# Kernel optimization log

Measured on AMD Instinct MI355X. Metric: run time of the kernel, lower is better.

## Reference

```python
import jax, jax.numpy as jnp
import numpy as np

B, L, D, E, V = 8, 256, 512, 64, 1000  # batch, length, input_size, edge_size, vocab


def setup_inputs() -> dict:
    key = jax.random.key(0)
    ks = jax.random.split(key, 16)
    s = 0.05
    inp = {
        "inputs": jax.random.normal(ks[0], (B, L, D), jnp.float32),
        "mains": jax.random.randint(ks[1], (B,), 0, L, jnp.int32),
        "adj1": jax.random.randint(ks[2], (B, L, L), 0, 2).astype(jnp.float32),
        "adj2": jax.random.randint(ks[3], (B, L, L), 0, 2).astype(jnp.float32),
        "edge1": jax.random.randint(ks[4], (B, L, L), 0, V, jnp.int32),
        "edge2": jax.random.randint(ks[5], (B, L, L), 0, V, jnp.int32),
        # parameters (torch Linear convention: W is (out, in), y = x @ W.T + b)
        "emb": jax.random.normal(ks[6], (V, E), jnp.float32) * s,
        "W1": jax.random.normal(ks[7], (E, D + E), jnp.float32) * s,
        "W2": jax.random.normal(ks[8], (D, D + E), jnp.float32) * s,
        "b2": jnp.zeros((D,), jnp.float32),
        "W3": jax.random.normal(ks[9], (E, D + E), jnp.float32) * s,
        "W4": jax.random.normal(ks[10], (D, D + E), jnp.float32) * s,
        "b4": jnp.zeros((D,), jnp.float32),
        "W5": jax.random.normal(ks[11], (D, 2 * D), jnp.float32) * s,
        "b5": jnp.zeros((D,), jnp.float32),
    }
    return inp


def reference(inputs, mains, adj1, adj2, edge1, edge2,
              emb, W1, W2, b2, W3, W4, b4, W5, b5):
    K = 3
    eps = 1e-10
    innum = jnp.sum(adj1 > 0, -1, keepdims=True).astype(inputs.dtype) + eps   # (B,L,1)
    outnum = jnp.sum(adj2 > 0, -1, keepdims=True).astype(inputs.dtype) + eps  # (B,L,1)

    # Edge contribution of sum(adj * cat([hid, edge]), -2) is iteration-invariant:
    # sum_j adj[b,i,j] * emb[edge[b,i,j]] -> compute once.
    e1 = emb[edge1]  # (B,L,L,E)
    e2 = emb[edge2]
    esum1 = jnp.einsum('bij,bije->bie', adj1, e1)  # (B,L,E)
    esum2 = jnp.einsum('bij,bije->bie', adj2, e2)

    hid1 = inputs
    hid2 = inputs
    for _ in range(K):
        # hid part of the masked neighbor sum: sum_j adj[b,i,j] * hid[b,j,:]
        hagg1 = jnp.einsum('bij,bjd->bid', adj1, hid1)                  # (B,L,D)
        agg1 = jnp.concatenate([hagg1, esum1], -1) / innum              # (B,L,D+E)
        h1e = jnp.tanh(agg1 @ W1.T)                                     # (B,L,E)
        hid1 = jnp.tanh(jnp.concatenate([h1e, hid1], -1) @ W2.T + b2)   # (B,L,D)

        hagg2 = jnp.einsum('bij,bjd->bid', adj2, hid2)
        agg2 = jnp.concatenate([hagg2, esum2], -1) / outnum
        h2e = jnp.tanh(agg2 @ W3.T)
        hid2 = jnp.tanh(jnp.concatenate([h2e, hid2], -1) @ W4.T + b4)

    fused = jnp.tanh(jnp.concatenate([hid1, hid2], -1) @ W5.T + b5)     # (B,L,D)
    return fused, fused[jnp.arange(fused.shape[0]), mains]
```

## Files before the change

### kernel.cpp

```cpp
#include <hip/hip_runtime.h>
#include <math.h>

#define B_  8
#define L_  256
#define D_  512
#define E_  64
#define DE_ 576
#define R_  2048
#define RG_ 4096

typedef unsigned short ushortT;
typedef __attribute__((ext_vector_type(8))) short bfrag;
typedef __attribute__((ext_vector_type(4))) float f32x4;

#define MFMA16(a,b,c) __builtin_amdgcn_mfma_f32_16x16x32_bf16(a,b,c,0,0,0)

__device__ inline ushortT f2bf(float x){
  unsigned u = __float_as_uint(x);
  u += 0x7FFFu + ((u >> 16) & 1u);
  return (ushortT)(u >> 16);
}
__device__ inline float bf2f(ushortT h){ return __uint_as_float(((unsigned)h) << 16); }

__global__ __launch_bounds__(256) void k_cvt(
    const float* __restrict__ W1, const float* __restrict__ W3,
    const float* __restrict__ W2, const float* __restrict__ W4,
    const float* __restrict__ W5,
    const float* __restrict__ adj1, const float* __restrict__ adj2,
    ushortT* W1h, ushortT* W1l, ushortT* W3h, ushortT* W3l,
    ushortT* W2h, ushortT* W2l, ushortT* W4h, ushortT* W4l,
    ushortT* W5h, ushortT* W5l, ushortT* adjb)
{
  const float* src; ushortT *dh, *dl; int n;
  switch (blockIdx.y) {
    case 0: src = W1;  dh = W1h; dl = W1l; n = 36864;  break;
    case 1: src = W3;  dh = W3h; dl = W3l; n = 36864;  break;
    case 2: src = W2;  dh = W2h; dl = W2l; n = 294912; break;
    case 3: src = W4;  dh = W4h; dl = W4l; n = 294912; break;
    case 4: src = W5;  dh = W5h; dl = W5l; n = 524288; break;
    case 5: src = adj1; dh = adjb;          dl = 0; n = 524288; break;
    default: src = adj2; dh = adjb + 524288; dl = 0; n = 524288; break;
  }
  int i4 = blockIdx.x * 256 + threadIdx.x;
  if (i4 * 4 >= n) return;
  float4 v = ((const float4*)src)[i4];
  float xs[4] = {v.x, v.y, v.z, v.w};
  ushortT h[4], lo[4];
  #pragma unroll
  for (int i = 0; i < 4; ++i) {
    h[i] = f2bf(xs[i]);
    lo[i] = f2bf(xs[i] - bf2f(h[i]));
  }
  ((ushort4*)dh)[i4] = make_ushort4(h[0], h[1], h[2], h[3]);
  if (dl) ((ushort4*)dl)[i4] = make_ushort4(lo[0], lo[1], lo[2], lo[3]);
}

__global__ __launch_bounds__(256) void k_precompute(
    const float* __restrict__ adj1, const float* __restrict__ adj2,
    const int* __restrict__ edge1, const int* __restrict__ edge2,
    const float* __restrict__ emb,
    ushortT* __restrict__ esumh, ushortT* __restrict__ esuml,
    float* __restrict__ num)
{
  int g = blockIdx.x >> 11;
  int r = blockIdx.x & 2047;
  const float* adj  = (g ? adj2 : adj1) + (size_t)r * L_;
  const int*   edge = (g ? edge2 : edge1) + (size_t)r * L_;
  const float4* emb4 = (const float4*)emb;

  int t = threadIdx.x;
  int e4 = t & 15, jc = t >> 4;
  float4 acc = {0.f, 0.f, 0.f, 0.f};
  float cnt = 0.f;
  #pragma unroll
  for (int k = 0; k < 16; ++k) {
    int j = jc * 16 + k;
    float a = adj[j];
    if (a != 0.0f) {
      int id = edge[j];
      float4 e = emb4[(size_t)id * 16 + e4];
      acc.x += a * e.x; acc.y += a * e.y; acc.z += a * e.z; acc.w += a * e.w;
      if (e4 == 0 && a > 0.0f) cnt += 1.0f;
    }
  }

  __shared__ float4 red[16][16];
  __shared__ float cred[16];
  red[jc][e4] = acc;
  if (e4 == 0) cred[jc] = cnt;
  __syncthreads();
  for (int s = 8; s > 0; s >>= 1) {
    if (jc < s) {
      float4 o = red[jc + s][e4];
      float4 m = red[jc][e4];
      m.x += o.x; m.y += o.y; m.z += o.z; m.w += o.w;
      red[jc][e4] = m;
    }
    __syncthreads();
  }
  if (t < 16) {
    float4 v = red[0][t];
    float xs[4] = {v.x, v.y, v.z, v.w};
    size_t base = ((size_t)g * R_ + r) * 64 + t * 4;
    #pragma unroll
    for (int i = 0; i < 4; ++i) {
      ushortT hi = f2bf(xs[i]);
      esumh[base + i] = hi;
      esuml[base + i] = f2bf(xs[i] - bf2f(hi));
    }
  }
  if (t == 0) {
    float c = 0.f;
    #pragma unroll
    for (int q = 0; q < 16; ++q) c += cred[q];
    num[g * R_ + r] = c + 1e-10f;
  }
}

__global__ __launch_bounds__(256) void k_init_hid(
    const float* __restrict__ inp, ushortT* __restrict__ hh, ushortT* __restrict__ hl)
{
  int idx = blockIdx.x * 256 + threadIdx.x;
  float4 v = ((const float4*)inp)[idx];
  float xs[4] = {v.x, v.y, v.z, v.w};
  ushortT h[4], lo[4];
  #pragma unroll
  for (int i = 0; i < 4; ++i) {
    h[i] = f2bf(xs[i]);
    lo[i] = f2bf(xs[i] - bf2f(h[i]));
  }
  ushort4 vh = make_ushort4(h[0], h[1], h[2], h[3]);
  ushort4 vl = make_ushort4(lo[0], lo[1], lo[2], lo[3]);
  ((ushort4*)hh)[idx] = vh;              ((ushort4*)hl)[idx] = vl;
  ((ushort4*)hh)[idx + 262144] = vh;     ((ushort4*)hl)[idx + 262144] = vl;
}

__global__ __launch_bounds__(256) void k_hagg(
    const ushortT* __restrict__ adjb,
    const ushortT* __restrict__ hidh, const ushortT* __restrict__ hidl,
    ushortT* __restrict__ hagh, ushortT* __restrict__ hagl)
{
  int bid = blockIdx.x;
  int batch = bid >> 5;
  int tile = bid & 31;
  int tm = tile >> 3, tn = tile & 7;
  int g = batch >> 3, b = batch & 7;
  const ushortT* A = adjb + (size_t)batch * 65536;
  size_t rowbase = (size_t)g * R_ + (size_t)b * L_;
  int c0 = tn * 64;

  __shared__ ushortT Blds[2][64][40];

  int t = threadIdx.x;
  int l = t & 63, w = t >> 6;
  int wm = (w >> 1) * 32, wn = (w & 1) * 32;
  int lg = l >> 4, l16 = l & 15;

  f32x4 z = {0.f, 0.f, 0.f, 0.f};
  f32x4 acc[2][2] = {{z, z}, {z, z}};

  int sj = t >> 3;
  int sq = t & 7;
  int sd0 = sq * 8;

  for (int kt = 0; kt < 8; ++kt) {
    size_t jglob = rowbase + kt * 32 + sj;
    bfrag vh = *(const bfrag*)(hidh + jglob * 512 + c0 + sd0);
    bfrag vl = *(const bfrag*)(hidl + jglob * 512 + c0 + sd0);
    #pragma unroll
    for (int i = 0; i < 8; ++i) {
      int ii = (i + sq) & 7;
      Blds[0][sd0 + ii][sj] = (ushortT)vh[ii];
      Blds[1][sd0 + ii][sj] = (ushortT)vl[ii];
    }
    __syncthreads();
    bfrag a0 = *(const bfrag*)(A + (size_t)(tm * 64 + wm + l16) * 256 + kt * 32 + 8 * lg);
    bfrag a1 = *(const bfrag*)(A + (size_t)(tm * 64 + wm + 16 + l16) * 256 + kt * 32 + 8 * lg);
    #pragma unroll
    for (int f = 0; f < 2; ++f) {
      bfrag bh = *(const bfrag*)&Blds[0][wn + 16 * f + l16][8 * lg];
      bfrag bl = *(const bfrag*)&Blds[1][wn + 16 * f + l16][8 * lg];
      acc[0][f] = MFMA16(a0, bh, acc[0][f]);
      acc[0][f] = MFMA16(a0, bl, acc[0][f]);
      acc[1][f] = MFMA16(a1, bh, acc[1][f]);
      acc[1][f] = MFMA16(a1, bl, acc[1][f]);
    }
    __syncthreads();
  }
  size_t orow0 = rowbase + tm * 64 + wm;
  #pragma unroll
  for (int e = 0; e < 2; ++e)
    #pragma unroll
    for (int f = 0; f < 2; ++f)
      #pragma unroll
      for (int j = 0; j < 4; ++j) {
        size_t row = orow0 + 16 * e + 4 * lg + j;
        int col = c0 + wn + 16 * f + l16;
        float x = acc[e][f][j];
        ushortT hi = f2bf(x);
        hagh[row * 512 + col] = hi;
        hagl[row * 512 + col] = f2bf(x - bf2f(hi));
      }
}

__global__ __launch_bounds__(64) void k_he(
    const ushortT* __restrict__ hagh, const ushortT* __restrict__ hagl,
    const ushortT* __restrict__ esumh, const ushortT* __restrict__ esuml,
    const float* __restrict__ num,
    const ushortT* __restrict__ W1h, const ushortT* __restrict__ W1l,
    const ushortT* __restrict__ W3h, const ushortT* __restrict__ W3l,
    ushortT* __restrict__ heh, ushortT* __restrict__ hel)
{
  int r0 = blockIdx.x * 16;
  int g = blockIdx.x >> 7;
  const ushortT* Wh = g ? W3h : W1h;
  const ushortT* Wl = g ? W3l : W1l;
  int l = threadIdx.x;
  int lg = l >> 4, l16 = l & 15;
  f32x4 z = {0.f, 0.f, 0.f, 0.f};
  f32x4 acc[4] = {z, z, z, z};
  size_t rA = r0 + l16;

  for (int kt = 0; kt < 18; ++kt) {
    const ushortT *sh, *sl; int stride, koff;
    if (kt < 16) { sh = hagh; sl = hagl; stride = 512; koff = kt * 32; }
    else         { sh = esumh; sl = esuml; stride = 64; koff = kt * 32 - 512; }
    int kk = koff + 8 * lg;
    bfrag ah = *(const bfrag*)(sh + rA * stride + kk);
    bfrag al = *(const bfrag*)(sl + rA * stride + kk);
    int kw = kt * 32 + 8 * lg;
    #pragma unroll
    for (int f = 0; f < 4; ++f) {
      bfrag bh = *(const bfrag*)(Wh + (size_t)(16 * f + l16) * DE_ + kw);
      bfrag bl = *(const bfrag*)(Wl + (size_t)(16 * f + l16) * DE_ + kw);
      acc[f] = MFMA16(ah, bh, acc[f]);
      acc[f] = MFMA16(ah, bl, acc[f]);
      acc[f] = MFMA16(al, bh, acc[f]);
    }
  }
  #pragma unroll
  for (int j = 0; j < 4; ++j) {
    size_t row = r0 + 4 * lg + j;
    float s = 1.0f / num[row];
    #pragma unroll
    for (int f = 0; f < 4; ++f) {
      float y = tanhf(acc[f][j] * s);
      int col = 16 * f + l16;
      ushortT hi = f2bf(y);
      heh[row * 64 + col] = hi;
      hel[row * 64 + col] = f2bf(y - bf2f(hi));
    }
  }
}

__global__ __launch_bounds__(256) void k_hid(
    const ushortT* __restrict__ heh, const ushortT* __restrict__ hel,
    const ushortT* __restrict__ hidh, const ushortT* __restrict__ hidl,
    const ushortT* __restrict__ W2h, const ushortT* __restrict__ W2l,
    const ushortT* __restrict__ W4h, const ushortT* __restrict__ W4l,
    const float* __restrict__ b2, const float* __restrict__ b4,
    ushortT* __restrict__ outh, ushortT* __restrict__ outl)
{
  int bm = blockIdx.x >> 3, bn = blockIdx.x & 7;
  int r0 = bm * 64, c0 = bn * 64;
  int g = bm >> 5;
  const ushortT* Wh = g ? W4h : W2h;
  const ushortT* Wl = g ? W4l : W2l;
  const float* bias = g ? b4 : b2;
  int t = threadIdx.x, l = t & 63, w = t >> 6;
  int wm = (w >> 1) * 32, wn = (w & 1) * 32;
  int lg = l >> 4, l16 = l & 15;
  f32x4 z = {0.f, 0.f, 0.f, 0.f};
  f32x4 acc[2][2] = {{z, z}, {z, z}};
  size_t rA0 = r0 + wm + l16;
  size_t nW0 = c0 + wn + l16;

  for (int kt = 0; kt < 18; ++kt) {
    const ushortT *sh, *sl; int stride, koff;
    if (kt < 2) { sh = heh; sl = hel; stride = 64; koff = kt * 32; }
    else        { sh = hidh; sl = hidl; stride = 512; koff = kt * 32 - 64; }
    int kk = koff + 8 * lg;
    bfrag a0h = *(const bfrag*)(sh + rA0 * stride + kk);
    bfrag a0l = *(const bfrag*)(sl + rA0 * stride + kk);
    bfrag a1h = *(const bfrag*)(sh + (rA0 + 16) * stride + kk);
    bfrag a1l = *(const bfrag*)(sl + (rA0 + 16) * stride + kk);
    int kw = kt * 32 + 8 * lg;
    bfrag b0h = *(const bfrag*)(Wh + nW0 * DE_ + kw);
    bfrag b0l = *(const bfrag*)(Wl + nW0 * DE_ + kw);
    bfrag b1h = *(const bfrag*)(Wh + (nW0 + 16) * DE_ + kw);
    bfrag b1l = *(const bfrag*)(Wl + (nW0 + 16) * DE_ + kw);
    acc[0][0] = MFMA16(a0h, b0h, acc[0][0]);
    acc[0][0] = MFMA16(a0h, b0l, acc[0][0]);
    acc[0][0] = MFMA16(a0l, b0h, acc[0][0]);
    acc[0][1] = MFMA16(a0h, b1h, acc[0][1]);
    acc[0][1] = MFMA16(a0h, b1l, acc[0][1]);
    acc[0][1] = MFMA16(a0l, b1h, acc[0][1]);
    acc[1][0] = MFMA16(a1h, b0h, acc[1][0]);
    acc[1][0] = MFMA16(a1h, b0l, acc[1][0]);
    acc[1][0] = MFMA16(a1l, b0h, acc[1][0]);
    acc[1][1] = MFMA16(a1h, b1h, acc[1][1]);
    acc[1][1] = MFMA16(a1h, b1l, acc[1][1]);
    acc[1][1] = MFMA16(a1l, b1h, acc[1][1]);
  }
  float bb[2] = {bias[nW0], bias[nW0 + 16]};
  #pragma unroll
  for (int e = 0; e < 2; ++e)
    #pragma unroll
    for (int f = 0; f < 2; ++f)
      #pragma unroll
      for (int j = 0; j < 4; ++j) {
        size_t row = r0 + wm + 16 * e + 4 * lg + j;
        int col = c0 + wn + 16 * f + l16;
        float y = tanhf(acc[e][f][j] + bb[f]);
        ushortT hi = f2bf(y);
        outh[row * 512 + col] = hi;
        outl[row * 512 + col] = f2bf(y - bf2f(hi));
      }
}

__global__ __launch_bounds__(256) void k_final(
    const ushortT* __restrict__ hidh, const ushortT* __restrict__ hidl,
    const ushortT* __restrict__ W5h, const ushortT* __restrict__ W5l,
    const float* __restrict__ b5, float* __restrict__ out)
{
  int bm = blockIdx.x >> 3, bn = blockIdx.x & 7;
  int r0 = bm * 64, c0 = bn * 64;
  int t = threadIdx.x, l = t & 63, w = t >> 6;
  int wm = (w >> 1) * 32, wn = (w & 1) * 32;
  int lg = l >> 4, l16 = l & 15;
  f32x4 z = {0.f, 0.f, 0.f, 0.f};
  f32x4 acc[2][2] = {{z, z}, {z, z}};
  size_t nW0 = c0 + wn + l16;

  for (int kt = 0; kt < 32; ++kt) {
    size_t rowoff = (kt < 16) ? 0 : (size_t)R_;
    int koff = (kt & 15) * 32;
    size_t rA0 = rowoff + r0 + wm + l16;
    int kk = koff + 8 * lg;
    bfrag a0h = *(const bfrag*)(hidh + rA0 * 512 + kk);
    bfrag a0l = *(const bfrag*)(hidl + rA0 * 512 + kk);
    bfrag a1h = *(const bfrag*)(hidh + (rA0 + 16) * 512 + kk);
    bfrag a1l = *(const bfrag*)(hidl + (rA0 + 16) * 512 + kk);
    int kw = kt * 32 + 8 * lg;
    bfrag b0h = *(const bfrag*)(W5h + nW0 * 1024 + kw);
    bfrag b0l = *(const bfrag*)(W5l + nW0 * 1024 + kw);
    bfrag b1h = *(const bfrag*)(W5h + (nW0 + 16) * 1024 + kw);
    bfrag b1l = *(const bfrag*)(W5l + (nW0 + 16) * 1024 + kw);
    acc[0][0] = MFMA16(a0h, b0h, acc[0][0]);
    acc[0][0] = MFMA16(a0h, b0l, acc[0][0]);
    acc[0][0] = MFMA16(a0l, b0h, acc[0][0]);
    acc[0][1] = MFMA16(a0h, b1h, acc[0][1]);
    acc[0][1] = MFMA16(a0h, b1l, acc[0][1]);
    acc[0][1] = MFMA16(a0l, b1h, acc[0][1]);
    acc[1][0] = MFMA16(a1h, b0h, acc[1][0]);
    acc[1][0] = MFMA16(a1h, b0l, acc[1][0]);
    acc[1][0] = MFMA16(a1l, b0h, acc[1][0]);
    acc[1][1] = MFMA16(a1h, b1h, acc[1][1]);
    acc[1][1] = MFMA16(a1h, b1l, acc[1][1]);
    acc[1][1] = MFMA16(a1l, b1h, acc[1][1]);
  }
  float bb[2] = {b5[nW0], b5[nW0 + 16]};
  #pragma unroll
  for (int e = 0; e < 2; ++e)
    #pragma unroll
    for (int f = 0; f < 2; ++f)
      #pragma unroll
      for (int j = 0; j < 4; ++j) {
        size_t row = r0 + wm + 16 * e + 4 * lg + j;
        int col = c0 + wn + 16 * f + l16;
        out[row * 512 + col] = tanhf(acc[e][f][j] + bb[f]);
      }
}

__global__ __launch_bounds__(512) void k_gather(
    const float* __restrict__ fused, const int* __restrict__ mains,
    float* __restrict__ out2)
{
  int b = blockIdx.x;
  int row = mains[b];
  out2[(size_t)b * D_ + threadIdx.x] =
      fused[((size_t)b * L_ + row) * D_ + threadIdx.x];
}

extern "C" void kernel_launch(void* const* d_in, const int* in_sizes, int n_in,
                              void* d_out, int out_size, void* d_ws, size_t ws_size,
                              hipStream_t stream)
{
  const float* inputs = (const float*)d_in[0];
  const int*   mains  = (const int*)d_in[1];
  const float* adj1   = (const float*)d_in[2];
  const float* adj2   = (const float*)d_in[3];
  const int*   edge1  = (const int*)d_in[4];
  const int*   edge2  = (const int*)d_in[5];
  const float* emb    = (const float*)d_in[6];
  const float* W1     = (const float*)d_in[7];
  const float* W2     = (const float*)d_in[8];
  const float* b2     = (const float*)d_in[9];
  const float* W3     = (const float*)d_in[10];
  const float* W4     = (const float*)d_in[11];
  const float* b4     = (const float*)d_in[12];
  const float* W5     = (const float*)d_in[13];
  const float* b5     = (const float*)d_in[14];
  float* out = (float*)d_out;

  char* p = (char*)d_ws;
  auto carve = [&](size_t bytes) { void* q = (void*)p; p += (bytes + 15) & ~(size_t)15; return q; };
  float*   num   = (float*)carve(4096 * 4);
  ushortT* esumh = (ushortT*)carve(262144 * 2);
  ushortT* esuml = (ushortT*)carve(262144 * 2);
  ushortT* adjb  = (ushortT*)carve(1048576 * 2);
  ushortT* W1h = (ushortT*)carve(36864 * 2),  *W1l = (ushortT*)carve(36864 * 2);
  ushortT* W3h = (ushortT*)carve(36864 * 2),  *W3l = (ushortT*)carve(36864 * 2);
  ushortT* W2h = (ushortT*)carve(294912 * 2), *W2l = (ushortT*)carve(294912 * 2);
  ushortT* W4h = (ushortT*)carve(294912 * 2), *W4l = (ushortT*)carve(294912 * 2);
  ushortT* W5h = (ushortT*)carve(524288 * 2), *W5l = (ushortT*)carve(524288 * 2);
  ushortT* heh = (ushortT*)carve(262144 * 2), *hel = (ushortT*)carve(262144 * 2);
  ushortT* H0h = (ushortT*)carve(2097152 * 2), *H0l = (ushortT*)carve(2097152 * 2);
  ushortT* H1h = (ushortT*)carve(2097152 * 2), *H1l = (ushortT*)carve(2097152 * 2);

  k_cvt<<<dim3(512, 7), 256, 0, stream>>>(W1, W3, W2, W4, W5, adj1, adj2,
      W1h, W1l, W3h, W3l, W2h, W2l, W4h, W4l, W5h, W5l, adjb);
  k_precompute<<<4096, 256, 0, stream>>>(adj1, adj2, edge1, edge2, emb, esumh, esuml, num);
  k_init_hid<<<1024, 256, 0, stream>>>(inputs, H0h, H0l);

  ushortT *ch = H0h, *cl = H0l, *oh = H1h, *ol = H1l;
  for (int it = 0; it < 3; ++it) {
    k_hagg<<<512, 256, 0, stream>>>(adjb, ch, cl, oh, ol);
    k_he<<<256, 64, 0, stream>>>(oh, ol, esumh, esuml, num, W1h, W1l, W3h, W3l, heh, hel);
    k_hid<<<512, 256, 0, stream>>>(heh, hel, ch, cl, W2h, W2l, W4h, W4l, b2, b4, oh, ol);
    ushortT* th = ch; ch = oh; oh = th;
    ushortT* tl = cl; cl = ol; ol = tl;
  }
  k_final<<<256, 256, 0, stream>>>(ch, cl, W5h, W5l, b5, out);
  k_gather<<<8, 512, 0, stream>>>(out, mains, out + (size_t)R_ * D_);
}
```

Measured before the change: 363.5 us.

## Reassociate adjacency aggregation: project hidden by W1/W3 before multiplying by adj

Uses associativity to compute Z = hid·W1[:, :512]^T (width 64) first, then adj·Z, instead of adj·hid (width 512) followed by the projection. This cuts the adjacency matmul from N=512 to N=64 and removes the full-width hagg intermediate write and read. Z is stored transposed so it can serve as the MFMA B operand. Rounding moves to the 64-wide Z in hi/lo bf16 form, which slightly changes numerics, and both new kernels use small single-wave blocks.

```diff
diff --git a/kernel.cpp b/kernel.cpp
--- a/kernel.cpp
+++ b/kernel.cpp
@@ -135,84 +135,14 @@
   ((ushort4*)hh)[idx + 262144] = vh;     ((ushort4*)hl)[idx + 262144] = vl;
 }
 
-__global__ __launch_bounds__(256) void k_hagg(
-    const ushortT* __restrict__ adjb,
+__global__ __launch_bounds__(64) void k_z(
     const ushortT* __restrict__ hidh, const ushortT* __restrict__ hidl,
-    ushortT* __restrict__ hagh, ushortT* __restrict__ hagl)
-{
-  int bid = blockIdx.x;
-  int batch = bid >> 5;
-  int tile = bid & 31;
-  int tm = tile >> 3, tn = tile & 7;
-  int g = batch >> 3, b = batch & 7;
-  const ushortT* A = adjb + (size_t)batch * 65536;
-  size_t rowbase = (size_t)g * R_ + (size_t)b * L_;
-  int c0 = tn * 64;
-
-  __shared__ ushortT Blds[2][64][40];
-
-  int t = threadIdx.x;
-  int l = t & 63, w = t >> 6;
-  int wm = (w >> 1) * 32, wn = (w & 1) * 32;
-  int lg = l >> 4, l16 = l & 15;
-
-  f32x4 z = {0.f, 0.f, 0.f, 0.f};
-  f32x4 acc[2][2] = {{z, z}, {z, z}};
-
-  int sj = t >> 3;
-  int sq = t & 7;
-  int sd0 = sq * 8;
-
-  for (int kt = 0; kt < 8; ++kt) {
-    size_t jglob = rowbase + kt * 32 + sj;
-    bfrag vh = *(const bfrag*)(hidh + jglob * 512 + c0 + sd0);
-    bfrag vl = *(const bfrag*)(hidl + jglob * 512 + c0 + sd0);
-    #pragma unroll
-    for (int i = 0; i < 8; ++i) {
-      int ii = (i + sq) & 7;
-      Blds[0][sd0 + ii][sj] = (ushortT)vh[ii];
-      Blds[1][sd0 + ii][sj] = (ushortT)vl[ii];
-    }
-    __syncthreads();
-    bfrag a0 = *(const bfrag*)(A + (size_t)(tm * 64 + wm + l16) * 256 + kt * 32 + 8 * lg);
-    bfrag a1 = *(const bfrag*)(A + (size_t)(tm * 64 + wm + 16 + l16) * 256 + kt * 32 + 8 * lg);
-    #pragma unroll
-    for (int f = 0; f < 2; ++f) {
-      bfrag bh = *(const bfrag*)&Blds[0][wn + 16 * f + l16][8 * lg];
-      bfrag bl = *(const bfrag*)&Blds[1][wn + 16 * f + l16][8 * lg];
-      acc[0][f] = MFMA16(a0, bh, acc[0][f]);
-      acc[0][f] = MFMA16(a0, bl, acc[0][f]);
-      acc[1][f] = MFMA16(a1, bh, acc[1][f]);
-      acc[1][f] = MFMA16(a1, bl, acc[1][f]);
-    }
-    __syncthreads();
-  }
-  size_t orow0 = rowbase + tm * 64 + wm;
-  #pragma unroll
-  for (int e = 0; e < 2; ++e)
-    #pragma unroll
-    for (int f = 0; f < 2; ++f)
-      #pragma unroll
-      for (int j = 0; j < 4; ++j) {
-        size_t row = orow0 + 16 * e + 4 * lg + j;
-        int col = c0 + wn + 16 * f + l16;
-        float x = acc[e][f][j];
-        ushortT hi = f2bf(x);
-        hagh[row * 512 + col] = hi;
-        hagl[row * 512 + col] = f2bf(x - bf2f(hi));
-      }
-}
-
-__global__ __launch_bounds__(64) void k_he(
-    const ushortT* __restrict__ hagh, const ushortT* __restrict__ hagl,
-    const ushortT* __restrict__ esumh, const ushortT* __restrict__ esuml,
-    const float* __restrict__ num,
     const ushortT* __restrict__ W1h, const ushortT* __restrict__ W1l,
     const ushortT* __restrict__ W3h, const ushortT* __restrict__ W3l,
-    ushortT* __restrict__ heh, ushortT* __restrict__ hel)
+    ushortT* __restrict__ zth, ushortT* __restrict__ ztl)
 {
   int r0 = blockIdx.x * 16;
-  int g = blockIdx.x >> 7;
+  int g = r0 >> 11;
   const ushortT* Wh = g ? W3h : W1h;
   const ushortT* Wl = g ? W3l : W1l;
   int l = threadIdx.x;
@@ -221,21 +151,76 @@
   f32x4 acc[4] = {z, z, z, z};
   size_t rA = r0 + l16;
 
-  for (int kt = 0; kt < 18; ++kt) {
-    const ushortT *sh, *sl; int stride, koff;
-    if (kt < 16) { sh = hagh; sl = hagl; stride = 512; koff = kt * 32; }
-    else         { sh = esumh; sl = esuml; stride = 64; koff = kt * 32 - 512; }
-    int kk = koff + 8 * lg;
-    bfrag ah = *(const bfrag*)(sh + rA * stride + kk);
-    bfrag al = *(const bfrag*)(sl + rA * stride + kk);
-    int kw = kt * 32 + 8 * lg;
+  for (int kt = 0; kt < 16; ++kt) {
+    int kk = kt * 32 + 8 * lg;
+    bfrag ah = *(const bfrag*)(hidh + rA * 512 + kk);
+    bfrag al = *(const bfrag*)(hidl + rA * 512 + kk);
     #pragma unroll
     for (int f = 0; f < 4; ++f) {
-      bfrag bh = *(const bfrag*)(Wh + (size_t)(16 * f + l16) * DE_ + kw);
-      bfrag bl = *(const bfrag*)(Wl + (size_t)(16 * f + l16) * DE_ + kw);
+      bfrag bh = *(const bfrag*)(Wh + (size_t)(16 * f + l16) * DE_ + kk);
+      bfrag bl = *(const bfrag*)(Wl + (size_t)(16 * f + l16) * DE_ + kk);
       acc[f] = MFMA16(ah, bh, acc[f]);
       acc[f] = MFMA16(ah, bl, acc[f]);
       acc[f] = MFMA16(al, bh, acc[f]);
+    }
+  }
+  #pragma unroll
+  for (int j = 0; j < 4; ++j) {
+    size_t row = r0 + 4 * lg + j;
+    #pragma unroll
+    for (int f = 0; f < 4; ++f) {
+      int col = 16 * f + l16;
+      float x = acc[f][j];
+      ushortT hi = f2bf(x);
+      zth[(size_t)col * RG_ + row] = hi;
+      ztl[(size_t)col * RG_ + row] = f2bf(x - bf2f(hi));
+    }
+  }
+}
+
+__global__ __launch_bounds__(64) void k_he2(
+    const ushortT* __restrict__ adjb,
+    const ushortT* __restrict__ zth, const ushortT* __restrict__ ztl,
+    const ushortT* __restrict__ esumh, const ushortT* __restrict__ esuml,
+    const float* __restrict__ num,
+    const ushortT* __restrict__ W1h, const ushortT* __restrict__ W1l,
+    const ushortT* __restrict__ W3h, const ushortT* __restrict__ W3l,
+    ushortT* __restrict__ heh, ushortT* __restrict__ hel)
+{
+  int r0 = blockIdx.x * 16;
+  int g = r0 >> 11;
+  int bt = r0 >> 8;
+  int rl = r0 & 255;
+  const ushortT* A = adjb + (size_t)bt * 65536;
+  const ushortT* Wh = g ? W3h : W1h;
+  const ushortT* Wl = g ? W3l : W1l;
+  int l = threadIdx.x;
+  int lg = l >> 4, l16 = l & 15;
+  f32x4 z = {0.f, 0.f, 0.f, 0.f};
+  f32x4 acc[4] = {z, z, z, z};
+
+  for (int kt = 0; kt < 8; ++kt) {
+    int kk = kt * 32 + 8 * lg;
+    bfrag a = *(const bfrag*)(A + (size_t)(rl + l16) * 256 + kk);
+    #pragma unroll
+    for (int f = 0; f < 4; ++f) {
+      bfrag zh_ = *(const bfrag*)(zth + (size_t)(16 * f + l16) * RG_ + bt * 256 + kk);
+      bfrag zl_ = *(const bfrag*)(ztl + (size_t)(16 * f + l16) * RG_ + bt * 256 + kk);
+      acc[f] = MFMA16(a, zh_, acc[f]);
+      acc[f] = MFMA16(a, zl_, acc[f]);
+    }
+  }
+  for (int kt = 0; kt < 2; ++kt) {
+    int kk = kt * 32 + 8 * lg;
+    bfrag eh = *(const bfrag*)(esumh + (size_t)(r0 + l16) * 64 + kk);
+    bfrag el = *(const bfrag*)(esuml + (size_t)(r0 + l16) * 64 + kk);
+    #pragma unroll
+    for (int f = 0; f < 4; ++f) {
+      bfrag wh = *(const bfrag*)(Wh + (size_t)(16 * f + l16) * DE_ + 512 + kk);
+      bfrag wl = *(const bfrag*)(Wl + (size_t)(16 * f + l16) * DE_ + 512 + kk);
+      acc[f] = MFMA16(eh, wh, acc[f]);
+      acc[f] = MFMA16(eh, wl, acc[f]);
+      acc[f] = MFMA16(el, wh, acc[f]);
     }
   }
   #pragma unroll
@@ -415,6 +400,7 @@
   ushortT* W4h = (ushortT*)carve(294912 * 2), *W4l = (ushortT*)carve(294912 * 2);
   ushortT* W5h = (ushortT*)carve(524288 * 2), *W5l = (ushortT*)carve(524288 * 2);
   ushortT* heh = (ushortT*)carve(262144 * 2), *hel = (ushortT*)carve(262144 * 2);
+  ushortT* zth = (ushortT*)carve(262144 * 2), *ztl = (ushortT*)carve(262144 * 2);
   ushortT* H0h = (ushortT*)carve(2097152 * 2), *H0l = (ushortT*)carve(2097152 * 2);
   ushortT* H1h = (ushortT*)carve(2097152 * 2), *H1l = (ushortT*)carve(2097152 * 2);
 
@@ -425,8 +411,9 @@
 
   ushortT *ch = H0h, *cl = H0l, *oh = H1h, *ol = H1l;
   for (int it = 0; it < 3; ++it) {
-    k_hagg<<<512, 256, 0, stream>>>(adjb, ch, cl, oh, ol);
-    k_he<<<256, 64, 0, stream>>>(oh, ol, esumh, esuml, num, W1h, W1l, W3h, W3l, heh, hel);
+    k_z<<<256, 64, 0, stream>>>(ch, cl, W1h, W1l, W3h, W3l, zth, ztl);
+    k_he2<<<256, 64, 0, stream>>>(adjb, zth, ztl, esumh, esuml, num,
+                                  W1h, W1l, W3h, W3l, heh, hel);
     k_hid<<<512, 256, 0, stream>>>(heh, hel, ch, cl, W2h, W2l, W4h, W4l, b2, b4, oh, ol);
     ushortT* th = ch; ch = oh; oh = th;
     ushortT* tl = cl; cl = ol; ol = tl;
```

After: 335.5 us. -7.7%, faster.
